# Performance work log

Hardware: AMD Instinct MI355X
Metric: run time of the kernel (lower is better)

The kernel has to match this reference:

```python
import jax, jax.numpy as jnp
import numpy as np

C = 64; H = 80; W = 160; B = 3; L = 4
REC = [4, 3, 2]  # agents per scene, sum = 9
EPS = 1e-5
NEG = -1e30  # stands in for -inf (numerically identical after softmax)


def setup_inputs() -> dict:
    key = jax.random.key(0)
    ks = jax.random.split(key, 24)
    def p(i, shape, s=0.05):
        return s * jax.random.normal(ks[i], shape, jnp.float32)
    x = jax.random.normal(ks[0], (sum(REC), C, H, W), jnp.float32)
    mask = jnp.ones((B, L, H, W), jnp.float32)
    record_len = jnp.array(REC, jnp.int32)
    eye = jnp.broadcast_to(jnp.array([[1., 0., 0.], [0., 1., 0.]], jnp.float32), (B, L, L, 2, 3))
    noise = 0.05 * jax.random.normal(ks[1], (B, L, L, 2, 3), jnp.float32)
    diag = jnp.eye(L, dtype=bool)[None, :, :, None, None]
    pairwise_t_matrix = jnp.where(diag, eye, eye + noise)  # near-identity normalized affines
    inp = dict(x=x, mask=mask, record_len=record_len, pairwise_t_matrix=pairwise_t_matrix)
    chans = [(2 * C, 128), (128, 32), (32, 8)]
    for n, (ci, co) in zip([1, 2, 3], chans):
        inp[f'w{n}'] = p(2 * n, (ci, co))
        inp[f'cb{n}'] = p(2 * n + 1, (co,), 0.01)
        inp[f'g{n}'] = 1.0 + p(8 + n, (co,), 0.1)
        inp[f'be{n}'] = p(12 + n, (co,), 0.1)
        inp[f'rm{n}'] = jnp.zeros((co,), jnp.float32)
        inp[f'rv{n}'] = jnp.ones((co,), jnp.float32)
    inp['w4'] = p(16, (8, 1)); inp['cb4'] = p(17, (1,), 0.01)
    inp['mlp_w'] = p(18, (C, C)); inp['mlp_b'] = p(19, (C,), 0.01)
    return inp


def _bilinear(feat, px, py):
    # feat [C,H,W]; px,py [H,W] source pixel coords; zero padding outside
    x0 = jnp.floor(px); y0 = jnp.floor(py)
    wx = px - x0; wy = py - y0
    x0i = x0.astype(jnp.int32); y0i = y0.astype(jnp.int32)
    def gat(xi, yi):
        inb = ((xi >= 0) & (xi < W) & (yi >= 0) & (yi < H)).astype(feat.dtype)
        v = feat[:, jnp.clip(yi, 0, H - 1), jnp.clip(xi, 0, W - 1)]
        return v * inb
    return (gat(x0i, y0i) * (1 - wx) * (1 - wy) + gat(x0i + 1, y0i) * wx * (1 - wy)
            + gat(x0i, y0i + 1) * (1 - wx) * wy + gat(x0i + 1, y0i + 1) * wx * wy)


def _warp_one(feat, theta):
    # torch affine_grid convention: src_norm = theta @ [x_n, y_n, 1]
    ys = jnp.linspace(-1.0, 1.0, H); xs = jnp.linspace(-1.0, 1.0, W)
    gx, gy = jnp.meshgrid(xs, ys)  # [H,W]
    sx = theta[0, 0] * gx + theta[0, 1] * gy + theta[0, 2]
    sy = theta[1, 0] * gx + theta[1, 1] * gy + theta[1, 2]
    px = (sx + 1.0) * (W - 1) / 2.0
    py = (sy + 1.0) * (H - 1) / 2.0
    return _bilinear(feat, px, py)

_warp_j = jax.vmap(_warp_one, in_axes=(0, 0))        # over neighbor j
_warp_ij = jax.vmap(_warp_j, in_axes=(None, 0))      # over ego i
_warp_bij = jax.vmap(_warp_ij, in_axes=(0, 0))       # over scene b


def _forward(x, mask, rec, ptm, w1, cb1, g1, be1, rm1, rv1, w2, cb2, g2, be2, rm2, rv2,
             w3, cb3, g3, be3, rm3, rv3, w4, cb4, mlp_w, mlp_b):
    # regroup: pad per-scene agent features to [B,L,C,H,W]
    feats, idx = [], 0
    for n in rec:
        feats.append(jnp.pad(x[idx:idx + n], ((0, L - n), (0, 0), (0, 0), (0, 0))))
        idx += n
    node = jnp.stack(feats)                                      # [B,L,C,H,W]
    valid = jnp.asarray((np.asarray(rec)[:, None] > np.arange(L)).astype(np.float32))  # [B,L]
    theta = jnp.swapaxes(ptm, 1, 2)                              # theta[b,i,j] = ptm[b,j,i]
    nbr = _warp_bij(node, theta)                                 # [B,L,L,C,H,W]
    wm = _warp_bij(mask[:, :, None], theta)                      # [B,L,L,1,H,W] warped ROI masks
    com_mask = wm * valid[:, None, :, None, None, None]
    ego = jnp.broadcast_to(node[:, :, None], nbr.shape)          # ego feature repeated over j
    z = jnp.concatenate([nbr, ego], axis=3)                      # [B,L,L,2C,H,W]

    def conv_bn_relu(t, w, cb, g, be, rm, rv):
        t = jnp.einsum('bijchw,co->bijohw', t, w) + cb[:, None, None]
        t = (t - rm[:, None, None]) * (g[:, None, None] / jnp.sqrt(rv[:, None, None] + EPS)) + be[:, None, None]
        return jax.nn.relu(t)

    h = conv_bn_relu(z, w1, cb1, g1, be1, rm1, rv1)
    h = conv_bn_relu(h, w2, cb2, g2, be2, rm2, rv2)
    h = conv_bn_relu(h, w3, cb3, g3, be3, rm3, rv3)
    s = jax.nn.relu(jnp.einsum('bijchw,co->bijohw', h, w4) + cb4[:, None, None])  # [B,L,L,1,H,W]
    s = jnp.where(com_mask == 0, NEG, s)
    aw = jax.nn.softmax(s, axis=2)                               # softmax over neighbors j
    updated = jnp.sum(aw * nbr * com_mask, axis=2)               # [B,L,C,H,W]
    out = updated[:, 0]                                          # ego agent per scene [B,C,H,W]
    return jnp.einsum('bchw,cd->bdhw', out, mlp_w) + mlp_b[:, None, None]


def reference(x, mask, record_len, pairwise_t_matrix, w1, cb1, g1, be1, rm1, rv1,
              w2, cb2, g2, be2, rm2, rv2, w3, cb3, g3, be3, rm3, rv3, w4, cb4, mlp_w, mlp_b):
    rec = [int(v) for v in np.asarray(record_len)]
    return _forward(x, mask, rec, pairwise_t_matrix, w1, cb1, g1, be1, rm1, rv1,
                    w2, cb2, g2, be2, rm2, rv2, w3, cb3, g3, be3, rm3, rv3, w4, cb4, mlp_w, mlp_b)
```

## Files before the change

### kernel.cpp

```cpp
#include <hip/hip_runtime.h>
#include <math.h>

#define CC 64
#define HH 80
#define WW 160
#define BB 3
#define LL 4
#define HW (HH * WW)
#define EPSf 1e-5f
#define NEGf -1e30f

typedef __attribute__((ext_vector_type(8))) short bf16x8;
typedef __attribute__((ext_vector_type(4))) float f32x4;

union BU { unsigned short s[8]; bf16x8 v; };

__device__ __forceinline__ unsigned short f2bf(float f) {
    unsigned int u = __float_as_uint(f);
    u = u + 0x7fffu + ((u >> 16) & 1u);
    return (unsigned short)(u >> 16);
}
__device__ __forceinline__ float b2f(unsigned short h) {
    return __uint_as_float(((unsigned int)h) << 16);
}

__device__ __forceinline__ void src_xy(const float* __restrict__ th, int pix,
                                       float& px, float& py) {
    int w = pix % WW, h = pix / WW;
    float gx = -1.f + 2.f * (float)w / (float)(WW - 1);
    float gy = -1.f + 2.f * (float)h / (float)(HH - 1);
    float sx = th[0] * gx + th[1] * gy + th[2];
    float sy = th[3] * gx + th[4] * gy + th[5];
    px = (sx + 1.f) * (float)(WW - 1) * 0.5f;
    py = (sy + 1.f) * (float)(HH - 1) * 0.5f;
}

struct Tap { int a00, a01, a10, a11; float w00, w01, w10, w11; };

__device__ __forceinline__ Tap mk_tap(float px, float py) {
    Tap tp;
    float x0f = floorf(px), y0f = floorf(py);
    float wx = px - x0f, wy = py - y0f;
    int x0 = (int)x0f, y0 = (int)y0f, x1 = x0 + 1, y1 = y0 + 1;
    float bx0 = (x0 >= 0 && x0 < WW) ? 1.f : 0.f;
    float bx1 = (x1 >= 0 && x1 < WW) ? 1.f : 0.f;
    float by0 = (y0 >= 0 && y0 < HH) ? 1.f : 0.f;
    float by1 = (y1 >= 0 && y1 < HH) ? 1.f : 0.f;
    int xc0 = min(max(x0, 0), WW - 1), xc1 = min(max(x1, 0), WW - 1);
    int yc0 = min(max(y0, 0), HH - 1), yc1 = min(max(y1, 0), HH - 1);
    tp.w00 = (1.f - wx) * (1.f - wy) * bx0 * by0;
    tp.w01 = wx * (1.f - wy) * bx1 * by0;
    tp.w10 = (1.f - wx) * wy * bx0 * by1;
    tp.w11 = wx * wy * bx1 * by1;
    tp.a00 = yc0 * WW + xc0; tp.a01 = yc0 * WW + xc1;
    tp.a10 = yc1 * WW + xc0; tp.a11 = yc1 * WW + xc1;
    return tp;
}


__global__ __launch_bounds__(256) void k_prep(
    const float* __restrict__ w1, const float* __restrict__ w2,
    const float* __restrict__ mlpw,
    const float* __restrict__ cb1, const float* __restrict__ g1,
    const float* __restrict__ be1, const float* __restrict__ rm1, const float* __restrict__ rv1,
    const float* __restrict__ cb2, const float* __restrict__ g2,
    const float* __restrict__ be2, const float* __restrict__ rm2, const float* __restrict__ rv2,
    const float* __restrict__ cb3, const float* __restrict__ g3,
    const float* __restrict__ be3, const float* __restrict__ rm3, const float* __restrict__ rv3,
    unsigned short* __restrict__ w1T, unsigned short* __restrict__ w2T,
    unsigned short* __restrict__ mwT,
    float* __restrict__ kk1, float* __restrict__ bb1,
    float* __restrict__ kk2, float* __restrict__ bb2,
    float* __restrict__ kk3, float* __restrict__ bb3)
{
    int idx = blockIdx.x * 256 + threadIdx.x;
    if (idx < 16384) {
        int o = idx >> 7, c = idx & 127;
        w1T[idx] = f2bf(w1[c * 128 + o]);
    } else if (idx < 20480) {
        int i = idx - 16384;
        int o2 = i >> 7, o = i & 127;
        w2T[i] = f2bf(w2[o * 32 + o2]);
    } else if (idx < 24576) {
        int i = idx - 20480;
        int d = i >> 6, c = i & 63;
        mwT[i] = f2bf(mlpw[c * 64 + d]);
    } else if (idx < 24704) {
        int o = idx - 24576;
        float k = g1[o] * rsqrtf(rv1[o] + EPSf);
        kk1[o] = k; bb1[o] = fmaf(cb1[o] - rm1[o], k, be1[o]);
    } else if (idx < 24736) {
        int o = idx - 24704;
        float k = g2[o] * rsqrtf(rv2[o] + EPSf);
        kk2[o] = k; bb2[o] = fmaf(cb2[o] - rm2[o], k, be2[o]);
    } else if (idx < 24744) {
        int o = idx - 24736;
        float k = g3[o] * rsqrtf(rv3[o] + EPSf);
        kk3[o] = k; bb3[o] = fmaf(cb3[o] - rm3[o], k, be3[o]);
    }
}


__global__ __launch_bounds__(256, 6) void k_fused(
    const float* __restrict__ x, const float* __restrict__ mask,
    const int* __restrict__ rec, const float* __restrict__ ptm,
    const unsigned short* __restrict__ w1T, const unsigned short* __restrict__ w2T,
    const unsigned short* __restrict__ mwT,
    const float* __restrict__ kk1, const float* __restrict__ bb1,
    const float* __restrict__ kk2, const float* __restrict__ bb2,
    const float* __restrict__ kk3, const float* __restrict__ bb3,
    const float* __restrict__ w3, const float* __restrict__ w4,
    const float* __restrict__ cb4, const float* __restrict__ mlp_b,
    float* __restrict__ out)
{
    __shared__ __align__(16) char pool[27136];
    unsigned short* nbr_s = (unsigned short*)pool;
    unsigned short* Hbase = (unsigned short*)(pool + 9216);
    unsigned short* ego_s = Hbase;
    float* s_s   = (float*)(pool + 26624);
    float* com_s = (float*)(pool + 26880);

    int t = threadIdx.x;
    int bid = blockIdx.x;
    int work = (bid & 7) * 300 + (bid >> 3);
    int b = work / 800, tile = work % 800;
    int pix0 = tile * 16;

    int wave = t >> 6, lane = t & 63, q = lane >> 4, r16 = lane & 15;

    int r0 = rec[0], r1 = rec[1], r2 = rec[2];
    int rb = (b == 0) ? r0 : ((b == 1) ? r1 : r2);
    int off = (b >= 1 ? r0 : 0) + (b >= 2 ? r1 : 0);
    bool validw = (wave < rb);

    {
        int pix = pix0 + r16;
        if (validw) {
            const float* th = ptm + (size_t)(b * 4 + wave) * 24;
            float fx, fy; src_xy(th, pix, fx, fy);
            Tap tp = mk_tap(fx, fy);
            if (q == 0) {
                const float* mk = mask + (size_t)(b * 4 + wave) * HW;
                float wm = tp.w00 * mk[tp.a00] + tp.w01 * mk[tp.a01]
                         + tp.w10 * mk[tp.a10] + tp.w11 * mk[tp.a11];
                com_s[wave * 16 + r16] = wm;
            }
            const float* feat = x + (size_t)(off + wave) * CC * HW;
            const float* p00 = feat + tp.a00;
            const float* p01 = feat + tp.a01;
            const float* p10 = feat + tp.a10;
            const float* p11 = feat + tp.a11;
            unsigned short* dst = nbr_s + (size_t)(wave * 16 + r16) * 72 + q * 16;
            #pragma unroll
            for (int i8 = 0; i8 < 2; ++i8) {
                float v00[8], v01[8], v10[8], v11[8];
                #pragma unroll
                for (int i = 0; i < 8; ++i) {
                    size_t co = (size_t)(q * 16 + i8 * 8 + i) * HW;
                    v00[i] = p00[co]; v01[i] = p01[co];
                    v10[i] = p10[co]; v11[i] = p11[co];
                }
                BU pk;
                #pragma unroll
                for (int i = 0; i < 8; ++i)
                    pk.s[i] = f2bf(tp.w00 * v00[i] + tp.w01 * v01[i]
                                 + tp.w10 * v10[i] + tp.w11 * v11[i]);
                *(bf16x8*)(dst + i8 * 8) = pk.v;
            }
        } else {
            bf16x8 zb = {0,0,0,0,0,0,0,0};
            unsigned short* dst = nbr_s + (size_t)(wave * 16 + r16) * 72 + q * 16;
            *(bf16x8*)(dst)     = zb;
            *(bf16x8*)(dst + 8) = zb;
            if (q == 0) { s_s[wave * 16 + r16] = NEGf; com_s[wave * 16 + r16] = 0.f; }
        }
        int pxe = t & 15, cg = t >> 4;
        const float* xe = x + (size_t)off * CC * HW + pix0 + pxe;
        unsigned short tmp[4];
        #pragma unroll
        for (int i = 0; i < 4; ++i)
            tmp[i] = f2bf(xe[(size_t)(cg * 4 + i) * HW]);
        *(uint2*)(ego_s + (size_t)pxe * 72 + cg * 4) = *(const uint2*)tmp;
    }
    __syncthreads();

    const f32x4 z4 = {0.f, 0.f, 0.f, 0.f};
    f32x4 acc1[8];
    #pragma unroll
    for (int nt = 0; nt < 8; ++nt) acc1[nt] = z4;
    {
        const unsigned short* nb = nbr_s + (size_t)(wave * 16) * 72;
        #pragma unroll
        for (int ks = 0; ks < 4; ++ks) {
            int kcol = (ks & 1) * 32 + q * 8;
            const unsigned short* base = (ks < 2) ? nb : ego_s;
            bf16x8 A = *(const bf16x8*)(base + (size_t)r16 * 72 + kcol);
            #pragma unroll
            for (int nt = 0; nt < 8; ++nt) {
                bf16x8 bw = *(const bf16x8*)(w1T + (size_t)(nt * 16 + r16) * 128
                                             + ks * 32 + q * 8);
                acc1[nt] = __builtin_amdgcn_mfma_f32_16x16x32_bf16(A, bw, acc1[nt], 0, 0, 0);
            }
        }
    }
    __syncthreads();

    if (validw) {
        unsigned short* H1w = Hbase + wave * (16 * 136);
        float* H2w = (float*)H1w;
        #pragma unroll
        for (int nt = 0; nt < 8; ++nt) {
            int o = nt * 16 + r16;
            float kv = kk1[o], bv = bb1[o];
            #pragma unroll
            for (int r = 0; r < 4; ++r) {
                float h = fmaxf(fmaf(acc1[nt][r], kv, bv), 0.f);
                H1w[(q * 4 + r) * 136 + o] = f2bf(h);
            }
        }
        f32x4 acc2[2]; acc2[0] = z4; acc2[1] = z4;
        #pragma unroll
        for (int ks = 0; ks < 4; ++ks) {
            int kcol = ks * 32 + q * 8;
            bf16x8 A = *(const bf16x8*)&H1w[r16 * 136 + kcol];
            #pragma unroll
            for (int nt = 0; nt < 2; ++nt) {
                bf16x8 bw = *(const bf16x8*)(w2T + (size_t)(nt * 16 + r16) * 128 + kcol);
                acc2[nt] = __builtin_amdgcn_mfma_f32_16x16x32_bf16(A, bw, acc2[nt], 0, 0, 0);
            }
        }
        #pragma unroll
        for (int nt = 0; nt < 2; ++nt) {
            int o = nt * 16 + r16;
            float kv = kk2[o], bv = bb2[o];
            #pragma unroll
            for (int r = 0; r < 4; ++r) {
                float h = fmaxf(fmaf(acc2[nt][r], kv, bv), 0.f);
                H2w[(q * 4 + r) * 36 + o] = h;
            }
        }
        if (q == 0) {
            float a3[8];
            #pragma unroll
            for (int o = 0; o < 8; ++o) a3[o] = 0.f;
            #pragma unroll 4
            for (int c = 0; c < 32; ++c) {
                float hv = H2w[r16 * 36 + c];
                #pragma unroll
                for (int o = 0; o < 8; ++o) a3[o] = fmaf(hv, w3[c * 8 + o], a3[o]);
            }
            float s = cb4[0];
            #pragma unroll
            for (int o = 0; o < 8; ++o) {
                float h = fmaxf(fmaf(a3[o], kk3[o], bb3[o]), 0.f);
                s = fmaf(h, w4[o], s);
            }
            s = fmaxf(s, 0.f);
            float wm = com_s[wave * 16 + r16];
            s_s[wave * 16 + r16] = (wm == 0.f) ? NEGf : s;
        }
    }
    __syncthreads();

    float sj[4], cj[4];
    #pragma unroll
    for (int j = 0; j < 4; ++j) { sj[j] = s_s[j * 16 + r16]; cj[j] = com_s[j * 16 + r16]; }
    float m = fmaxf(fmaxf(sj[0], sj[1]), fmaxf(sj[2], sj[3]));
    float e[4], sum = 0.f;
    #pragma unroll
    for (int j = 0; j < 4; ++j) { e[j] = __expf(sj[j] - m); sum += e[j]; }
    float inv = 1.f / sum;
    float wgt[4];
    #pragma unroll
    for (int j = 0; j < 4; ++j) wgt[j] = e[j] * inv * cj[j];

    float uf0[8], uf1[8];
    #pragma unroll
    for (int i = 0; i < 8; ++i) { uf0[i] = 0.f; uf1[i] = 0.f; }
    #pragma unroll
    for (int j = 0; j < 4; ++j) {
        float wj = wgt[j];
        bf16x8 n0 = *(const bf16x8*)&nbr_s[(size_t)(j * 16 + r16) * 72 + q * 8];
        bf16x8 n1 = *(const bf16x8*)&nbr_s[(size_t)(j * 16 + r16) * 72 + 32 + q * 8];
        #pragma unroll
        for (int i = 0; i < 8; ++i) {
            uf0[i] = fmaf(wj, b2f((unsigned short)n0[i]), uf0[i]);
            uf1[i] = fmaf(wj, b2f((unsigned short)n1[i]), uf1[i]);
        }
    }
    BU p0, p1;
    #pragma unroll
    for (int i = 0; i < 8; ++i) { p0.s[i] = f2bf(uf0[i]); p1.s[i] = f2bf(uf1[i]); }

    f32x4 acc3 = z4;
    #pragma unroll
    for (int ks = 0; ks < 2; ++ks) {
        bf16x8 A = ks ? p1.v : p0.v;
        bf16x8 bw = *(const bf16x8*)(mwT + (size_t)(wave * 16 + r16) * 64
                                     + ks * 32 + q * 8);
        acc3 = __builtin_amdgcn_mfma_f32_16x16x32_bf16(A, bw, acc3, 0, 0, 0);
    }
    __syncthreads();

    float* outT = (float*)pool;
    {
        int d = wave * 16 + r16;
        float mb = mlp_b[d];
        #pragma unroll
        for (int r = 0; r < 4; ++r)
            outT[d * 20 + q * 4 + r] = acc3[r] + mb;
    }
    __syncthreads();
    {
        int d = t >> 2, c4 = (t & 3) * 4;
        float4 v = *(const float4*)&outT[d * 20 + c4];
        *(float4*)&out[((size_t)(b * CC + d)) * HW + pix0 + c4] = v;
    }
}


extern "C" void kernel_launch(void* const* d_in, const int* in_sizes, int n_in,
                              void* d_out, int out_size, void* d_ws, size_t ws_size,
                              hipStream_t stream)
{
    const float* x    = (const float*)d_in[0];
    const float* mask = (const float*)d_in[1];
    const int*   rec  = (const int*)  d_in[2];
    const float* ptm  = (const float*)d_in[3];
    const float* w1   = (const float*)d_in[4];
    const float* cb1  = (const float*)d_in[5];
    const float* g1   = (const float*)d_in[6];
    const float* be1  = (const float*)d_in[7];
    const float* rm1  = (const float*)d_in[8];
    const float* rv1  = (const float*)d_in[9];
    const float* w2   = (const float*)d_in[10];
    const float* cb2  = (const float*)d_in[11];
    const float* g2   = (const float*)d_in[12];
    const float* be2  = (const float*)d_in[13];
    const float* rm2  = (const float*)d_in[14];
    const float* rv2  = (const float*)d_in[15];
    const float* w3   = (const float*)d_in[16];
    const float* cb3  = (const float*)d_in[17];
    const float* g3   = (const float*)d_in[18];
    const float* be3  = (const float*)d_in[19];
    const float* rm3  = (const float*)d_in[20];
    const float* rv3  = (const float*)d_in[21];
    const float* w4   = (const float*)d_in[22];
    const float* cb4  = (const float*)d_in[23];
    const float* mlpw = (const float*)d_in[24];
    const float* mlpb = (const float*)d_in[25];
    float* out = (float*)d_out;

    unsigned short* w1T = (unsigned short*)d_ws;
    unsigned short* w2T = w1T + 16384;
    unsigned short* mwT = w2T + 4096;
    float* kk1 = (float*)(mwT + 4096);
    float* bb1 = kk1 + 128;
    float* kk2 = bb1 + 128;
    float* bb2 = kk2 + 32;
    float* kk3 = bb2 + 32;
    float* bb3 = kk3 + 8;

    k_prep<<<dim3(97), dim3(256), 0, stream>>>(
        w1, w2, mlpw, cb1, g1, be1, rm1, rv1, cb2, g2, be2, rm2, rv2,
        cb3, g3, be3, rm3, rv3, w1T, w2T, mwT, kk1, bb1, kk2, bb2, kk3, bb3);

    k_fused<<<dim3(2400), dim3(256), 0, stream>>>(
        x, mask, rec, ptm, w1T, w2T, mwT,
        kk1, bb1, kk2, bb2, kk3, bb3,
        w3, w4, cb4, mlpb, out);
}
```

Before: 181.2 us.

## Pre-transpose features to pixel-major bf16 and gather bilinear taps as vectors

A preprocessing pass converts the input feature maps to a channel-last bf16 copy in workspace. The fused kernel can then load each bilinear tap's channels with contiguous 16-byte loads instead of channel-strided scalar fp32 loads. Layer-1 MMA operands, including the ego features, now stay in registers instead of going through shared memory, which removes a barrier. The cost is an extra full read and write pass over the input and a lower occupancy hint.

```diff
diff --git a/kernel.cpp b/kernel.cpp
--- a/kernel.cpp
+++ b/kernel.cpp
@@ -57,8 +57,18 @@
     return tp;
 }
 
-
-__global__ __launch_bounds__(256) void k_prep(
+__device__ __forceinline__ void blend8(uint4 v, float w, float* ac) {
+    unsigned uu[4] = {v.x, v.y, v.z, v.w};
+    #pragma unroll
+    for (int k = 0; k < 4; ++k) {
+        ac[2 * k + 0] = fmaf(w, __uint_as_float(uu[k] << 16),          ac[2 * k + 0]);
+        ac[2 * k + 1] = fmaf(w, __uint_as_float(uu[k] & 0xffff0000u), ac[2 * k + 1]);
+    }
+}
+
+
+__global__ __launch_bounds__(256) void k_pre(
+    const float* __restrict__ x,
     const float* __restrict__ w1, const float* __restrict__ w2,
     const float* __restrict__ mlpw,
     const float* __restrict__ cb1, const float* __restrict__ g1,
@@ -67,13 +77,33 @@
     const float* __restrict__ be2, const float* __restrict__ rm2, const float* __restrict__ rv2,
     const float* __restrict__ cb3, const float* __restrict__ g3,
     const float* __restrict__ be3, const float* __restrict__ rm3, const float* __restrict__ rv3,
+    unsigned short* __restrict__ xT,
     unsigned short* __restrict__ w1T, unsigned short* __restrict__ w2T,
     unsigned short* __restrict__ mwT,
     float* __restrict__ kk1, float* __restrict__ bb1,
     float* __restrict__ kk2, float* __restrict__ bb2,
     float* __restrict__ kk3, float* __restrict__ bb3)
 {
-    int idx = blockIdx.x * 256 + threadIdx.x;
+    int bid = blockIdx.x, t = threadIdx.x;
+    if (bid < 450) {
+        __shared__ unsigned short T[256 * 72];
+        int n = bid / 50, tile = bid % 50, px0 = tile * 256;
+        const float* src = x + (size_t)n * CC * HW + px0;
+        #pragma unroll 8
+        for (int c = 0; c < 64; ++c)
+            T[t * 72 + c] = f2bf(src[(size_t)c * HW + t]);
+        __syncthreads();
+        unsigned short* dst = xT + ((size_t)n * HW + px0) * 64;
+        #pragma unroll
+        for (int w = 0; w < 2; ++w) {
+            int idx = w * 256 + t, px = idx >> 1, hf = idx & 1;
+            const uint4* s = (const uint4*)&T[px * 72 + hf * 32];
+            uint4* d = (uint4*)(dst + (size_t)px * 64 + hf * 32);
+            d[0] = s[0]; d[1] = s[1]; d[2] = s[2]; d[3] = s[3];
+        }
+        return;
+    }
+    int idx = (bid - 450) * 256 + t;
     if (idx < 16384) {
         int o = idx >> 7, c = idx & 127;
         w1T[idx] = f2bf(w1[c * 128 + o]);
@@ -101,8 +131,8 @@
 }
 
 
-__global__ __launch_bounds__(256, 6) void k_fused(
-    const float* __restrict__ x, const float* __restrict__ mask,
+__global__ __launch_bounds__(256, 4) void k_fused(
+    const unsigned short* __restrict__ xT, const float* __restrict__ mask,
     const int* __restrict__ rec, const float* __restrict__ ptm,
     const unsigned short* __restrict__ w1T, const unsigned short* __restrict__ w2T,
     const unsigned short* __restrict__ mwT,
@@ -116,7 +146,6 @@
     __shared__ __align__(16) char pool[27136];
     unsigned short* nbr_s = (unsigned short*)pool;
     unsigned short* Hbase = (unsigned short*)(pool + 9216);
-    unsigned short* ego_s = Hbase;
     float* s_s   = (float*)(pool + 26624);
     float* com_s = (float*)(pool + 26880);
 
@@ -127,83 +156,71 @@
     int pix0 = tile * 16;
 
     int wave = t >> 6, lane = t & 63, q = lane >> 4, r16 = lane & 15;
+    int pix = pix0 + r16;
+    int q8 = q * 8;
 
     int r0 = rec[0], r1 = rec[1], r2 = rec[2];
     int rb = (b == 0) ? r0 : ((b == 1) ? r1 : r2);
     int off = (b >= 1 ? r0 : 0) + (b >= 2 ? r1 : 0);
     bool validw = (wave < rb);
 
-    {
-        int pix = pix0 + r16;
-        if (validw) {
-            const float* th = ptm + (size_t)(b * 4 + wave) * 24;
-            float fx, fy; src_xy(th, pix, fx, fy);
-            Tap tp = mk_tap(fx, fy);
-            if (q == 0) {
-                const float* mk = mask + (size_t)(b * 4 + wave) * HW;
-                float wm = tp.w00 * mk[tp.a00] + tp.w01 * mk[tp.a01]
-                         + tp.w10 * mk[tp.a10] + tp.w11 * mk[tp.a11];
-                com_s[wave * 16 + r16] = wm;
-            }
-            const float* feat = x + (size_t)(off + wave) * CC * HW;
-            const float* p00 = feat + tp.a00;
-            const float* p01 = feat + tp.a01;
-            const float* p10 = feat + tp.a10;
-            const float* p11 = feat + tp.a11;
-            unsigned short* dst = nbr_s + (size_t)(wave * 16 + r16) * 72 + q * 16;
-            #pragma unroll
-            for (int i8 = 0; i8 < 2; ++i8) {
-                float v00[8], v01[8], v10[8], v11[8];
-                #pragma unroll
-                for (int i = 0; i < 8; ++i) {
-                    size_t co = (size_t)(q * 16 + i8 * 8 + i) * HW;
-                    v00[i] = p00[co]; v01[i] = p01[co];
-                    v10[i] = p10[co]; v11[i] = p11[co];
-                }
-                BU pk;
-                #pragma unroll
-                for (int i = 0; i < 8; ++i)
-                    pk.s[i] = f2bf(tp.w00 * v00[i] + tp.w01 * v01[i]
-                                 + tp.w10 * v10[i] + tp.w11 * v11[i]);
-                *(bf16x8*)(dst + i8 * 8) = pk.v;
-            }
-        } else {
-            bf16x8 zb = {0,0,0,0,0,0,0,0};
-            unsigned short* dst = nbr_s + (size_t)(wave * 16 + r16) * 72 + q * 16;
-            *(bf16x8*)(dst)     = zb;
-            *(bf16x8*)(dst + 8) = zb;
-            if (q == 0) { s_s[wave * 16 + r16] = NEGf; com_s[wave * 16 + r16] = 0.f; }
-        }
-        int pxe = t & 15, cg = t >> 4;
-        const float* xe = x + (size_t)off * CC * HW + pix0 + pxe;
-        unsigned short tmp[4];
-        #pragma unroll
-        for (int i = 0; i < 4; ++i)
-            tmp[i] = f2bf(xe[(size_t)(cg * 4 + i) * HW]);
-        *(uint2*)(ego_s + (size_t)pxe * 72 + cg * 4) = *(const uint2*)tmp;
-    }
-    __syncthreads();
+    const unsigned short* egoT = xT + ((size_t)off * HW + pix) * 64;
+    bf16x8 e0 = *(const bf16x8*)(egoT + q8);
+    bf16x8 e1 = *(const bf16x8*)(egoT + 32 + q8);
+
+    bf16x8 A0, A1;
+    if (validw) {
+        const float* th = ptm + (size_t)(b * 4 + wave) * 24;
+        float fx, fy; src_xy(th, pix, fx, fy);
+        Tap tp = mk_tap(fx, fy);
+        if (q == 0) {
+            const float* mk = mask + (size_t)(b * 4 + wave) * HW;
+            float wm = tp.w00 * mk[tp.a00] + tp.w01 * mk[tp.a01]
+                     + tp.w10 * mk[tp.a10] + tp.w11 * mk[tp.a11];
+            com_s[wave * 16 + r16] = wm;
+        }
+        const unsigned short* fT = xT + (size_t)(off + wave) * HW * 64;
+        uint4 LA0 = *(const uint4*)(fT + (size_t)tp.a00 * 64 + q8);
+        uint4 LA1 = *(const uint4*)(fT + (size_t)tp.a00 * 64 + 32 + q8);
+        uint4 LB0 = *(const uint4*)(fT + (size_t)tp.a01 * 64 + q8);
+        uint4 LB1 = *(const uint4*)(fT + (size_t)tp.a01 * 64 + 32 + q8);
+        uint4 LC0 = *(const uint4*)(fT + (size_t)tp.a10 * 64 + q8);
+        uint4 LC1 = *(const uint4*)(fT + (size_t)tp.a10 * 64 + 32 + q8);
+        uint4 LD0 = *(const uint4*)(fT + (size_t)tp.a11 * 64 + q8);
+        uint4 LD1 = *(const uint4*)(fT + (size_t)tp.a11 * 64 + 32 + q8);
+        float ac0[8], ac1[8];
+        #pragma unroll
+        for (int i = 0; i < 8; ++i) { ac0[i] = 0.f; ac1[i] = 0.f; }
+        blend8(LA0, tp.w00, ac0); blend8(LA1, tp.w00, ac1);
+        blend8(LB0, tp.w01, ac0); blend8(LB1, tp.w01, ac1);
+        blend8(LC0, tp.w10, ac0); blend8(LC1, tp.w10, ac1);
+        blend8(LD0, tp.w11, ac0); blend8(LD1, tp.w11, ac1);
+        BU u0, u1;
+        #pragma unroll
+        for (int i = 0; i < 8; ++i) { u0.s[i] = f2bf(ac0[i]); u1.s[i] = f2bf(ac1[i]); }
+        A0 = u0.v; A1 = u1.v;
+    } else {
+        bf16x8 zb = {0,0,0,0,0,0,0,0};
+        A0 = zb; A1 = zb;
+        if (q == 0) { s_s[wave * 16 + r16] = NEGf; com_s[wave * 16 + r16] = 0.f; }
+    }
+    *(bf16x8*)&nbr_s[(size_t)(wave * 16 + r16) * 72 + q8]      = A0;
+    *(bf16x8*)&nbr_s[(size_t)(wave * 16 + r16) * 72 + 32 + q8] = A1;
 
     const f32x4 z4 = {0.f, 0.f, 0.f, 0.f};
     f32x4 acc1[8];
     #pragma unroll
     for (int nt = 0; nt < 8; ++nt) acc1[nt] = z4;
-    {
-        const unsigned short* nb = nbr_s + (size_t)(wave * 16) * 72;
-        #pragma unroll
-        for (int ks = 0; ks < 4; ++ks) {
-            int kcol = (ks & 1) * 32 + q * 8;
-            const unsigned short* base = (ks < 2) ? nb : ego_s;
-            bf16x8 A = *(const bf16x8*)(base + (size_t)r16 * 72 + kcol);
-            #pragma unroll
-            for (int nt = 0; nt < 8; ++nt) {
-                bf16x8 bw = *(const bf16x8*)(w1T + (size_t)(nt * 16 + r16) * 128
-                                             + ks * 32 + q * 8);
-                acc1[nt] = __builtin_amdgcn_mfma_f32_16x16x32_bf16(A, bw, acc1[nt], 0, 0, 0);
-            }
-        }
-    }
-    __syncthreads();
+    #pragma unroll
+    for (int ks = 0; ks < 4; ++ks) {
+        bf16x8 A = (ks == 0) ? A0 : (ks == 1) ? A1 : (ks == 2) ? e0 : e1;
+        #pragma unroll
+        for (int nt = 0; nt < 8; ++nt) {
+            bf16x8 bw = *(const bf16x8*)(w1T + (size_t)(nt * 16 + r16) * 128
+                                         + ks * 32 + q8);
+            acc1[nt] = __builtin_amdgcn_mfma_f32_16x16x32_bf16(A, bw, acc1[nt], 0, 0, 0);
+        }
+    }
 
     if (validw) {
         unsigned short* H1w = Hbase + wave * (16 * 136);
@@ -221,7 +238,7 @@
         f32x4 acc2[2]; acc2[0] = z4; acc2[1] = z4;
         #pragma unroll
         for (int ks = 0; ks < 4; ++ks) {
-            int kcol = ks * 32 + q * 8;
+            int kcol = ks * 32 + q8;
             bf16x8 A = *(const bf16x8*)&H1w[r16 * 136 + kcol];
             #pragma unroll
             for (int nt = 0; nt < 2; ++nt) {
@@ -280,8 +297,8 @@
     #pragma unroll
     for (int j = 0; j < 4; ++j) {
         float wj = wgt[j];
-        bf16x8 n0 = *(const bf16x8*)&nbr_s[(size_t)(j * 16 + r16) * 72 + q * 8];
-        bf16x8 n1 = *(const bf16x8*)&nbr_s[(size_t)(j * 16 + r16) * 72 + 32 + q * 8];
+        bf16x8 n0 = *(const bf16x8*)&nbr_s[(size_t)(j * 16 + r16) * 72 + q8];
+        bf16x8 n1 = *(const bf16x8*)&nbr_s[(size_t)(j * 16 + r16) * 72 + 32 + q8];
         #pragma unroll
         for (int i = 0; i < 8; ++i) {
             uf0[i] = fmaf(wj, b2f((unsigned short)n0[i]), uf0[i]);
@@ -296,8 +313,7 @@
     #pragma unroll
     for (int ks = 0; ks < 2; ++ks) {
         bf16x8 A = ks ? p1.v : p0.v;
-        bf16x8 bw = *(const bf16x8*)(mwT + (size_t)(wave * 16 + r16) * 64
-                                     + ks * 32 + q * 8);
+        bf16x8 bw = *(const bf16x8*)(mwT + (size_t)(wave * 16 + r16) * 64 + ks * 32 + q8);
         acc3 = __builtin_amdgcn_mfma_f32_16x16x32_bf16(A, bw, acc3, 0, 0, 0);
     }
     __syncthreads();
@@ -351,7 +367,8 @@
     const float* mlpb = (const float*)d_in[25];
     float* out = (float*)d_out;
 
-    unsigned short* w1T = (unsigned short*)d_ws;
+    unsigned short* xT  = (unsigned short*)d_ws;
+    unsigned short* w1T = xT + (size_t)9 * HW * 64;
     unsigned short* w2T = w1T + 16384;
     unsigned short* mwT = w2T + 4096;
     float* kk1 = (float*)(mwT + 4096);
@@ -361,12 +378,12 @@
     float* kk3 = bb2 + 32;
     float* bb3 = kk3 + 8;
 
-    k_prep<<<dim3(97), dim3(256), 0, stream>>>(
-        w1, w2, mlpw, cb1, g1, be1, rm1, rv1, cb2, g2, be2, rm2, rv2,
-        cb3, g3, be3, rm3, rv3, w1T, w2T, mwT, kk1, bb1, kk2, bb2, kk3, bb3);
+    k_pre<<<dim3(547), dim3(256), 0, stream>>>(
+        x, w1, w2, mlpw, cb1, g1, be1, rm1, rv1, cb2, g2, be2, rm2, rv2,
+        cb3, g3, be3, rm3, rv3, xT, w1T, w2T, mwT, kk1, bb1, kk2, bb2, kk3, bb3);
 
     k_fused<<<dim3(2400), dim3(256), 0, stream>>>(
-        x, mask, rec, ptm, w1T, w2T, mwT,
+        xT, mask, rec, ptm, w1T, w2T, mwT,
         kk1, bb1, kk2, bb2, kk3, bb3,
         w3, w4, cb4, mlpb, out);
 }
```

New measurement: 187.0 us. 3.2% more time.
